# Kernel tuning notes

Measured on AMD Instinct MI355X. Metric: run time of the kernel, lower is better.

The kernel has to match this reference:

```python
import jax, jax.numpy as jnp
import numpy as np

B, L, D, K = 4, 512, 768, 96
H = 4 * D  # projection hidden width


def _proj(x, w1, b1, w2, b2):
    # create_projection_layer: Linear -> ReLU -> (Dropout, identity at eval) -> Linear
    return jnp.maximum(x @ w1 + b1, 0.0) @ w2 + b2


def setup_inputs() -> dict:
    key = jax.random.key(0)
    ks = jax.random.split(key, 12)
    g = lambda k, shape, fan: jax.random.normal(k, shape, jnp.float32) * (1.0 / np.sqrt(fan))
    inp = {
        "h": jax.random.normal(ks[0], (B, L, D), jnp.float32),
        "span_idx": jax.random.randint(ks[1], (B, K, 2), 0, L),
        "ps_w1": g(ks[2], (D, H), D), "ps_b1": jnp.zeros((H,), jnp.float32),
        "ps_w2": g(ks[3], (H, D), H), "ps_b2": jnp.zeros((D,), jnp.float32),
        "pe_w1": g(ks[4], (D, H), D), "pe_b1": jnp.zeros((H,), jnp.float32),
        "pe_w2": g(ks[5], (H, D), H), "pe_b2": jnp.zeros((D,), jnp.float32),
        "so_w1": g(ks[6], (2 * D, H), 2 * D), "so_b1": jnp.zeros((H,), jnp.float32),
        "so_w2": g(ks[7], (H, D), H), "so_b2": jnp.zeros((D,), jnp.float32),
        "ro_w1": g(ks[8], (2 * D, H), 2 * D), "ro_b1": jnp.zeros((H,), jnp.float32),
        "ro_w2": g(ks[9], (H, D), H), "ro_b2": jnp.zeros((D,), jnp.float32),
    }
    return inp


def _gather_tokens(rep, idx):
    # rep: [B,L,D], idx: [B,K] -> [B,K,D]
    b, k = idx.shape
    d = rep.shape[-1]
    return jnp.take_along_axis(rep, jnp.broadcast_to(idx[:, :, None], (b, k, d)), axis=1)


def reference(h, span_idx, ps_w1, ps_b1, ps_w2, ps_b2, pe_w1, pe_b1, pe_w2, pe_b2,
              so_w1, so_b1, so_w2, so_b2, ro_w1, ro_b1, ro_w2, ro_b2):
    # SpanMarkerV1
    start_rep = _proj(h, ps_w1, ps_b1, ps_w2, ps_b2)   # [B,L,D]
    end_rep = _proj(h, pe_w1, pe_b1, pe_w2, pe_b2)     # [B,L,D]
    st = _gather_tokens(start_rep, span_idx[:, :, 0])  # [B,K,D]
    en = _gather_tokens(end_rep, span_idx[:, :, 1])    # [B,K,D]
    cat = jnp.maximum(jnp.concatenate([st, en], axis=-1), 0.0)  # relu
    entity_reps = _proj(cat, so_w1, so_b1, so_w2, so_b2)        # [B,K,D]

    # off-diagonal pair enumeration, row-major (i,j) with i != j — static indices
    n = entity_reps.shape[1]
    idx = np.arange(n)
    ii = np.repeat(idx, n)
    jj = np.tile(idx, n)
    keep = ii != jj
    ii, jj = ii[keep], jj[keep]  # each length n*(n-1)
    pairs = jnp.concatenate([entity_reps[:, ii], entity_reps[:, jj]], axis=-1)  # [B,P,2D]
    return _proj(pairs, ro_w1, ro_b1, ro_w2, ro_b2)  # [B,P,D]
```

## Files before the change

### kernel.cpp

```cpp
#include <hip/hip_runtime.h>
#include <hip/hip_bf16.h>

#define Bdim 4
#define Ldim 512
#define Ddim 768
#define Kspan 96
#define Hdim 3072
#define Pdim 9120
#define MROWS 384
#define NT6 96

typedef __bf16 bf16x8 __attribute__((ext_vector_type(8)));
typedef float f32x4 __attribute__((ext_vector_type(4)));
typedef float f32x16 __attribute__((ext_vector_type(16)));
typedef unsigned short ushort8v __attribute__((ext_vector_type(8)));
typedef unsigned int uint4v __attribute__((ext_vector_type(4)));

static __device__ __forceinline__ unsigned short f2bf(float x){
  return __builtin_bit_cast(unsigned short, (__bf16)x);
}
static __device__ __forceinline__ float bf2f(unsigned short u){
  return (float)__builtin_bit_cast(__bf16, u);
}

struct TJob { const float* W; unsigned short* Th; unsigned short* Tl; int K; int N; int base; };
struct TJobs { TJob j[7]; };

__global__ __launch_bounds__(256) void transpose_multi(TJobs JJ)
{
  int x = blockIdx.x;
  int ji = 0;
  #pragma unroll
  for (int q = 1; q < 7; q++) if (x >= JJ.j[q].base) ji = q;
  TJob J = JJ.j[ji];
  int local = x - J.base;
  int tilesX = J.N >> 6;
  int bx = local % tilesX, by = local / tilesX;
  __shared__ float tile[64][65];
  int k0 = by * 64, n0 = bx * 64;
  int c = threadIdx.x & 63, r0 = threadIdx.x >> 6;
  for (int p = 0; p < 16; p++){
    int r = r0 + p * 4;
    tile[c][r] = J.W[(size_t)(k0 + r) * J.N + n0 + c];
  }
  __syncthreads();
  for (int p = 0; p < 16; p++){
    int n = r0 + p * 4;
    float xv = tile[n][c];
    unsigned short h = f2bf(xv);
    size_t o = (size_t)(n0 + n) * J.K + k0 + c;
    J.Th[o] = h;
    J.Tl[o] = f2bf(xv - bf2f(h));
  }
}

__global__ __launch_bounds__(256) void pack_w2(
    const float* __restrict__ W, unsigned short* __restrict__ W2B)
{
  __shared__ float tile[32][129];
  int kt = blockIdx.x, nq = blockIdx.y, t = threadIdx.x;
  for (int q = 0; q < 16; q++){
    int flat = q * 256 + t;
    int kl = flat >> 7, n = flat & 127;
    tile[kl][n] = W[(size_t)(kt * 32 + kl) * Ddim + nq * 128 + n];
  }
  __syncthreads();
  unsigned short* outp = W2B + (size_t)(nq * 96 + kt) * 4096;
  for (int q = 0; q < 16; q++){
    int o = q * 256 + t;
    int wn = (o >> 11) & 1, kh = (o >> 10) & 1, nf = (o >> 9) & 1;
    int hs = (o >> 8) & 1, l31 = (o >> 3) & 31, e = o & 7;
    int nl = wn * 64 + nf * 32 + l31;
    int kl = (kh * 2 + hs) * 8 + e;
    outp[o] = f2bf(tile[kl][nl]);
  }
}

__global__ __launch_bounds__(256) void pack_v_frag(
    const unsigned short* __restrict__ Vb, unsigned short* __restrict__ Vpk)
{
  int kt = blockIdx.x, b = blockIdx.y, t = threadIdx.x;
  unsigned short* outp = Vpk + (size_t)(b * 96 + kt) * 3072;
  #pragma unroll
  for (int q = 0; q < 12; q++){
    int o = q * 256 + t;
    int kh = o / 1536;
    int rem = o - kh * 1536;
    int mf = rem >> 9;
    int rem2 = rem & 511;
    int hsel = rem2 >> 8, l31 = (rem2 >> 3) & 31, e = rem2 & 7;
    outp[o] = Vb[(size_t)(b * 96 + mf * 32 + l31) * Hdim + kt * 32 + (kh * 2 + hsel) * 8 + e];
  }
}

__global__ __launch_bounds__(256) void gather_rows(
    const float* __restrict__ h, const int* __restrict__ span, float* __restrict__ hg)
{
  int x = blockIdx.x;
  int sel = (x >= MROWS) ? 1 : 0;
  int r = x - sel * MROWS;
  int b = r / Kspan, k = r - b * Kspan;
  int idx = span[(b * Kspan + k) * 2 + sel];
  const float* src = h + ((size_t)b * Ldim + idx) * Ddim;
  float* dst = hg + (size_t)x * Ddim;
  for (int d = threadIdx.x; d < Ddim; d += 256) dst[d] = src[d];
}

struct GJob {
  const float* A;
  const unsigned short* Wh;
  const unsigned short* Wl;
  const float* bias;
  float* C;
};

template<int MODE, int SPLIT>
__global__ __launch_bounds__(256) void gemm_ms(
    GJob j0, GJob j1, int ldA, int ldW, int ldC, int kLen, size_t csz)
{
  constexpr int SR = 40;
  __shared__ __align__(16) unsigned short Ah[64 * SR], Al[64 * SR];
  __shared__ __align__(16) unsigned short Bh[128 * SR], Bl[128 * SR];
  int zj, s;
  if (SPLIT == 1){ zj = blockIdx.z; s = 0; }
  else { zj = blockIdx.z / SPLIT; s = blockIdx.z % SPLIT; }
  const GJob J = zj ? j1 : j0;
  int kBegin = s * kLen;
  float* Cptr = (MODE == 2) ? (J.C + (size_t)s * csz) : J.C;

  int m0 = blockIdx.y * 64, n0 = blockIdx.x * 128;
  int t = threadIdx.x, lane = t & 63, wid = t >> 6;
  int wm = wid >> 1, wn = wid & 1;
  int lr = lane & 15, lk = (lane >> 4) * 8;
  f32x4 acc[2][4] = {};
  int ar = t >> 2, akq = t & 3;
  for (int k0 = 0; k0 < kLen; k0 += 32){
    {
      const float* sp = J.A + (size_t)(m0 + ar) * ldA + kBegin + k0 + akq * 8;
      f32x4 x0 = *(const f32x4*)sp, x1 = *(const f32x4*)(sp + 4);
      ushort8v vh, vl;
      for (int e = 0; e < 4; e++){ float x = x0[e]; unsigned short hh = f2bf(x); vh[e] = hh; vl[e] = f2bf(x - bf2f(hh)); }
      for (int e = 0; e < 4; e++){ float x = x1[e]; unsigned short hh = f2bf(x); vh[e+4] = hh; vl[e+4] = f2bf(x - bf2f(hh)); }
      *(ushort8v*)&Ah[ar * SR + akq * 8] = vh;
      *(ushort8v*)&Al[ar * SR + akq * 8] = vl;
    }
    for (int p = 0; p < 2; p++){
      int idx = p * 256 + t; int n = idx >> 2, kq = idx & 3;
      size_t go = (size_t)(n0 + n) * ldW + kBegin + k0 + kq * 8;
      *(ushort8v*)&Bh[n * SR + kq * 8] = *(const ushort8v*)(J.Wh + go);
      *(ushort8v*)&Bl[n * SR + kq * 8] = *(const ushort8v*)(J.Wl + go);
    }
    __syncthreads();
    bf16x8 ah[2], al2[2], bh[4], bl[4];
    for (int f = 0; f < 2; f++){ int o = (wm * 32 + f * 16 + lr) * SR + lk; ah[f] = *(const bf16x8*)&Ah[o]; al2[f] = *(const bf16x8*)&Al[o]; }
    for (int g = 0; g < 4; g++){ int o = (wn * 64 + g * 16 + lr) * SR + lk; bh[g] = *(const bf16x8*)&Bh[o]; bl[g] = *(const bf16x8*)&Bl[o]; }
    for (int f = 0; f < 2; f++)
      for (int g = 0; g < 4; g++){
        acc[f][g] = __builtin_amdgcn_mfma_f32_16x16x32_bf16(ah[f],  bh[g], acc[f][g], 0, 0, 0);
        acc[f][g] = __builtin_amdgcn_mfma_f32_16x16x32_bf16(ah[f],  bl[g], acc[f][g], 0, 0, 0);
        acc[f][g] = __builtin_amdgcn_mfma_f32_16x16x32_bf16(al2[f], bh[g], acc[f][g], 0, 0, 0);
      }
    __syncthreads();
  }
  int rr = (lane >> 4) * 4;
  for (int f = 0; f < 2; f++){
    int gm = m0 + wm * 32 + f * 16 + rr;
    for (int g = 0; g < 4; g++){
      int gn = n0 + wn * 64 + g * 16 + (lane & 15);
      float bv = (MODE != 2 && J.bias) ? J.bias[gn] : 0.f;
      for (int r2 = 0; r2 < 4; r2++){
        float v = acc[f][g][r2] + bv;
        if (MODE == 0) v = fmaxf(v, 0.f);
        if (MODE == 6){
          ((unsigned short*)J.C)[(size_t)(gm + r2) * ldC + gn] = f2bf(v);
        } else {
          Cptr[(size_t)(gm + r2) * ldC + gn] = v;
        }
      }
    }
  }
}

template<bool RELU>
__global__ __launch_bounds__(256) void reduce_part(
    const float* __restrict__ P, int S,
    const float* __restrict__ bias0, const float* __restrict__ bias1,
    float* __restrict__ outp, int zCount, int ldOut)
{
  const int MN = MROWS * Ddim;
  int idx4 = blockIdx.x * 256 + threadIdx.x;
  int flat = idx4 * 4;
  if (flat >= MN * zCount) return;
  int z = flat / MN; int rem = flat - z * MN;
  int r = rem / Ddim; int c = rem - r * Ddim;
  const float* base = P + (size_t)z * S * MN + rem;
  f32x4 sv = *(const f32x4*)base;
  for (int ss = 1; ss < S; ss++){ f32x4 v = *(const f32x4*)(base + (size_t)ss * MN); sv += v; }
  const float* bp = z ? bias1 : bias0;
  f32x4 bv = *(const f32x4*)(bp + c);
  sv += bv;
  if (RELU) for (int e = 0; e < 4; e++) sv[e] = fmaxf(sv[e], 0.f);
  *(f32x4*)(outp + (size_t)r * ldOut + z * Ddim + c) = sv;
}

__global__ __launch_bounds__(256, 2) void pair_gemm13(
    const unsigned short* __restrict__ Ub,
    const unsigned short* __restrict__ Vpk,
    const unsigned short* __restrict__ W2B,
    const float* __restrict__ b2,
    float* __restrict__ out)
{
  int x = blockIdx.x;
  int xcd = x & 7;
  int s = x >> 3;
  int grp = s / 48;
  int ig  = s - grp * 48;
  int combo = xcd + grp * 8;
  int nq = combo % 6, b = combo / 6;

  int t = threadIdx.x, lane = t & 63, w = t >> 6;
  int wm = w >> 1, wn = w & 1;
  int l31 = lane & 31, hsel = lane >> 5;
  int i = ig * 2 + wm;

  f32x16 acc[3][2] = {};

  const unsigned short* Vt = Vpk + (size_t)(b * 96) * 3072 + lane * 8;
  const unsigned short* Wt = W2B + (size_t)(nq * 96) * 4096 + wn * 2048 + lane * 8;
  const unsigned short* Ut = Ub + (size_t)(b * 96 + i) * Hdim + hsel * 8;

  ushort8v vE0, vE1, vE2, vE3, vE4, vE5, uE0, uE1;
  ushort8v vO0, vO1, vO2, vO3, vO4, vO5, uO0, uO1;

  #define LOADV_(KT, V0, V1, V2, V3, V4, V5) { \
    const unsigned short* p_ = Vt + (size_t)(KT) * 3072; \
    V0 = *(const ushort8v*)(p_);        V1 = *(const ushort8v*)(p_ + 512); \
    V2 = *(const ushort8v*)(p_ + 1024); V3 = *(const ushort8v*)(p_ + 1536); \
    V4 = *(const ushort8v*)(p_ + 2048); V5 = *(const ushort8v*)(p_ + 2560); \
  }
  #define LOADU_(KT, U0, U1) { \
    const unsigned short* p_ = Ut + (KT) * 32; \
    U0 = *(const ushort8v*)(p_); U1 = *(const ushort8v*)(p_ + 16); \
  }

  auto mkfrag = [](ushort8v v, ushort8v u) -> bf16x8 {
    bf16x8 sv2 = __builtin_bit_cast(bf16x8, v) + __builtin_bit_cast(bf16x8, u);
    bf16x8 z = {};
    return __builtin_elementwise_max(sv2, z);
  };

  LOADV_(0, vE0, vE1, vE2, vE3, vE4, vE5);
  LOADU_(0, uE0, uE1);

  for (int kt = 0; kt < NT6; kt += 2){
    {
      const unsigned short* wp = Wt + (size_t)kt * 4096;
      ushort8v b0 = *(const ushort8v*)(wp);
      ushort8v b1 = *(const ushort8v*)(wp + 512);
      ushort8v b2v = *(const ushort8v*)(wp + 1024);
      ushort8v b3 = *(const ushort8v*)(wp + 1536);
      LOADV_(kt + 1, vO0, vO1, vO2, vO3, vO4, vO5);
      LOADU_(kt + 1, uO0, uO1);
      bf16x8 a;
      a = mkfrag(vE0, uE0);
      acc[0][0] = __builtin_amdgcn_mfma_f32_32x32x16_bf16(a, __builtin_bit_cast(bf16x8, b0), acc[0][0], 0, 0, 0);
      acc[0][1] = __builtin_amdgcn_mfma_f32_32x32x16_bf16(a, __builtin_bit_cast(bf16x8, b1), acc[0][1], 0, 0, 0);
      a = mkfrag(vE1, uE0);
      acc[1][0] = __builtin_amdgcn_mfma_f32_32x32x16_bf16(a, __builtin_bit_cast(bf16x8, b0), acc[1][0], 0, 0, 0);
      acc[1][1] = __builtin_amdgcn_mfma_f32_32x32x16_bf16(a, __builtin_bit_cast(bf16x8, b1), acc[1][1], 0, 0, 0);
      a = mkfrag(vE2, uE0);
      acc[2][0] = __builtin_amdgcn_mfma_f32_32x32x16_bf16(a, __builtin_bit_cast(bf16x8, b0), acc[2][0], 0, 0, 0);
      acc[2][1] = __builtin_amdgcn_mfma_f32_32x32x16_bf16(a, __builtin_bit_cast(bf16x8, b1), acc[2][1], 0, 0, 0);
      a = mkfrag(vE3, uE1);
      acc[0][0] = __builtin_amdgcn_mfma_f32_32x32x16_bf16(a, __builtin_bit_cast(bf16x8, b2v), acc[0][0], 0, 0, 0);
      acc[0][1] = __builtin_amdgcn_mfma_f32_32x32x16_bf16(a, __builtin_bit_cast(bf16x8, b3), acc[0][1], 0, 0, 0);
      a = mkfrag(vE4, uE1);
      acc[1][0] = __builtin_amdgcn_mfma_f32_32x32x16_bf16(a, __builtin_bit_cast(bf16x8, b2v), acc[1][0], 0, 0, 0);
      acc[1][1] = __builtin_amdgcn_mfma_f32_32x32x16_bf16(a, __builtin_bit_cast(bf16x8, b3), acc[1][1], 0, 0, 0);
      a = mkfrag(vE5, uE1);
      acc[2][0] = __builtin_amdgcn_mfma_f32_32x32x16_bf16(a, __builtin_bit_cast(bf16x8, b2v), acc[2][0], 0, 0, 0);
      acc[2][1] = __builtin_amdgcn_mfma_f32_32x32x16_bf16(a, __builtin_bit_cast(bf16x8, b3), acc[2][1], 0, 0, 0);
    }
    {
      int ko = kt + 1;
      const unsigned short* wp = Wt + (size_t)ko * 4096;
      ushort8v b0 = *(const ushort8v*)(wp);
      ushort8v b1 = *(const ushort8v*)(wp + 512);
      ushort8v b2v = *(const ushort8v*)(wp + 1024);
      ushort8v b3 = *(const ushort8v*)(wp + 1536);
      if (ko + 1 < NT6){
        LOADV_(ko + 1, vE0, vE1, vE2, vE3, vE4, vE5);
        LOADU_(ko + 1, uE0, uE1);
      }
      bf16x8 a;
      a = mkfrag(vO0, uO0);
      acc[0][0] = __builtin_amdgcn_mfma_f32_32x32x16_bf16(a, __builtin_bit_cast(bf16x8, b0), acc[0][0], 0, 0, 0);
      acc[0][1] = __builtin_amdgcn_mfma_f32_32x32x16_bf16(a, __builtin_bit_cast(bf16x8, b1), acc[0][1], 0, 0, 0);
      a = mkfrag(vO1, uO0);
      acc[1][0] = __builtin_amdgcn_mfma_f32_32x32x16_bf16(a, __builtin_bit_cast(bf16x8, b0), acc[1][0], 0, 0, 0);
      acc[1][1] = __builtin_amdgcn_mfma_f32_32x32x16_bf16(a, __builtin_bit_cast(bf16x8, b1), acc[1][1], 0, 0, 0);
      a = mkfrag(vO2, uO0);
      acc[2][0] = __builtin_amdgcn_mfma_f32_32x32x16_bf16(a, __builtin_bit_cast(bf16x8, b0), acc[2][0], 0, 0, 0);
      acc[2][1] = __builtin_amdgcn_mfma_f32_32x32x16_bf16(a, __builtin_bit_cast(bf16x8, b1), acc[2][1], 0, 0, 0);
      a = mkfrag(vO3, uO1);
      acc[0][0] = __builtin_amdgcn_mfma_f32_32x32x16_bf16(a, __builtin_bit_cast(bf16x8, b2v), acc[0][0], 0, 0, 0);
      acc[0][1] = __builtin_amdgcn_mfma_f32_32x32x16_bf16(a, __builtin_bit_cast(bf16x8, b3), acc[0][1], 0, 0, 0);
      a = mkfrag(vO4, uO1);
      acc[1][0] = __builtin_amdgcn_mfma_f32_32x32x16_bf16(a, __builtin_bit_cast(bf16x8, b2v), acc[1][0], 0, 0, 0);
      acc[1][1] = __builtin_amdgcn_mfma_f32_32x32x16_bf16(a, __builtin_bit_cast(bf16x8, b3), acc[1][1], 0, 0, 0);
      a = mkfrag(vO5, uO1);
      acc[2][0] = __builtin_amdgcn_mfma_f32_32x32x16_bf16(a, __builtin_bit_cast(bf16x8, b2v), acc[2][0], 0, 0, 0);
      acc[2][1] = __builtin_amdgcn_mfma_f32_32x32x16_bf16(a, __builtin_bit_cast(bf16x8, b3), acc[2][1], 0, 0, 0);
    }
  }
  #undef LOADV_
  #undef LOADU_

  size_t outB = (size_t)b * Pdim;
  int colbase = nq * 128 + wn * 64;
  float bc[2];
  #pragma unroll
  for (int nf = 0; nf < 2; nf++) bc[nf] = b2[colbase + nf * 32 + l31];
  #pragma unroll
  for (int mf = 0; mf < 3; mf++){
    #pragma unroll
    for (int reg = 0; reg < 16; reg++){
      int j = mf * 32 + (reg & 3) + 8 * (reg >> 2) + 4 * hsel;
      if (j == i) continue;
      int p = i * 95 + j - (j > i ? 1 : 0);
      float* orow = out + (outB + p) * Ddim + colbase;
      #pragma unroll
      for (int nf = 0; nf < 2; nf++)
        orow[nf * 32 + l31] = acc[mf][nf][reg] + bc[nf];
    }
  }
}

extern "C" void kernel_launch(void* const* d_in, const int* in_sizes, int n_in,
                              void* d_out, int out_size, void* d_ws, size_t ws_size,
                              hipStream_t stream)
{
  (void)in_sizes; (void)n_in; (void)out_size;
  const float* h     = (const float*)d_in[0];
  const int*   span  = (const int*)d_in[1];
  const float* ps_w1 = (const float*)d_in[2];
  const float* ps_b1 = (const float*)d_in[3];
  const float* ps_w2 = (const float*)d_in[4];
  const float* ps_b2 = (const float*)d_in[5];
  const float* pe_w1 = (const float*)d_in[6];
  const float* pe_b1 = (const float*)d_in[7];
  const float* pe_w2 = (const float*)d_in[8];
  const float* pe_b2 = (const float*)d_in[9];
  const float* so_w1 = (const float*)d_in[10];
  const float* so_b1 = (const float*)d_in[11];
  const float* so_w2 = (const float*)d_in[12];
  const float* so_b2 = (const float*)d_in[13];
  const float* ro_w1 = (const float*)d_in[14];
  const float* ro_b1 = (const float*)d_in[15];
  const float* ro_w2 = (const float*)d_in[16];
  const float* ro_b2 = (const float*)d_in[17];

  char* ws = (char*)d_ws;
  size_t off = 0;
  auto alloc_us = [&](size_t n)->unsigned short*{
    unsigned short* p = (unsigned short*)(ws + off);
    off += ((n * 2 + 255) & ~(size_t)255);
    return p;
  };
  auto alloc_f = [&](size_t n)->float*{
    float* p = (float*)(ws + off);
    off += ((n * 4 + 255) & ~(size_t)255);
    return p;
  };

  unsigned short* ps1h = alloc_us((size_t)Hdim * Ddim); unsigned short* ps1l = alloc_us((size_t)Hdim * Ddim);
  unsigned short* ps2h = alloc_us((size_t)Ddim * Hdim); unsigned short* ps2l = alloc_us((size_t)Ddim * Hdim);
  unsigned short* pe1h = alloc_us((size_t)Hdim * Ddim); unsigned short* pe1l = alloc_us((size_t)Hdim * Ddim);
  unsigned short* pe2h = alloc_us((size_t)Ddim * Hdim); unsigned short* pe2l = alloc_us((size_t)Ddim * Hdim);
  unsigned short* so1h = alloc_us((size_t)Hdim * 2 * Ddim); unsigned short* so1l = alloc_us((size_t)Hdim * 2 * Ddim);
  unsigned short* so2h = alloc_us((size_t)Ddim * Hdim); unsigned short* so2l = alloc_us((size_t)Ddim * Hdim);
  unsigned short* ro1h = alloc_us((size_t)Hdim * 2 * Ddim); unsigned short* ro1l = alloc_us((size_t)Hdim * 2 * Ddim);
  unsigned short* W2B  = alloc_us((size_t)6 * 96 * 4096);
  unsigned short* Vp   = alloc_us((size_t)MROWS * Hdim);
  unsigned short* Ubf  = alloc_us((size_t)MROWS * Hdim);
  unsigned short* Vpk  = alloc_us((size_t)MROWS * Hdim);
  float* hg     = alloc_f((size_t)2 * MROWS * Ddim);
  float* mid_s  = alloc_f((size_t)MROWS * Hdim);
  float* mid_e  = alloc_f((size_t)MROWS * Hdim);
  float* cat    = alloc_f((size_t)MROWS * 2 * Ddim);
  float* entity = alloc_f((size_t)MROWS * Ddim);
  const size_t MN = (size_t)MROWS * Ddim;
  float* P2 = alloc_f(8 * MN);
  float* P3 = alloc_f(8 * MN);
  if (off > ws_size) return;

  dim3 tb(256);

  {
    TJobs JJ;
    int base = 0;
    auto add = [&](int idx, const float* W, unsigned short* Th, unsigned short* Tl, int K, int N){
      JJ.j[idx] = TJob{W, Th, Tl, K, N, base};
      base += (N / 64) * (K / 64);
    };
    add(0, ps_w1, ps1h, ps1l, Ddim, Hdim);
    add(1, ps_w2, ps2h, ps2l, Hdim, Ddim);
    add(2, pe_w1, pe1h, pe1l, Ddim, Hdim);
    add(3, pe_w2, pe2h, pe2l, Hdim, Ddim);
    add(4, so_w1, so1h, so1l, 2 * Ddim, Hdim);
    add(5, so_w2, so2h, so2l, Hdim, Ddim);
    add(6, ro_w1, ro1h, ro1l, 2 * Ddim, Hdim);
    transpose_multi<<<base, tb, 0, stream>>>(JJ);
  }
  pack_w2<<<dim3(NT6, 6), tb, 0, stream>>>(ro_w2, W2B);

  gather_rows<<<2 * MROWS, tb, 0, stream>>>(h, span, hg);

  {
    GJob j0{hg,                      ps1h, ps1l, ps_b1, mid_s};
    GJob j1{hg + (size_t)MROWS*Ddim, pe1h, pe1l, pe_b1, mid_e};
    gemm_ms<0,1><<<dim3(Hdim/128, MROWS/64, 2), tb, 0, stream>>>(j0, j1, Ddim, Ddim, Hdim, Ddim, 0);
  }
  {
    GJob j0{mid_s, ps2h, ps2l, nullptr, P2};
    GJob j1{mid_e, pe2h, pe2l, nullptr, P2 + 4*MN};
    gemm_ms<2,4><<<dim3(Ddim/128, MROWS/64, 8), tb, 0, stream>>>(j0, j1, Hdim, Hdim, Ddim, Hdim/4, MN);
  }
  reduce_part<true><<<(2*(int)MN)/1024, tb, 0, stream>>>(P2, 4, ps_b2, pe_b2, cat, 2, 2*Ddim);
  {
    GJob j0{cat, so1h, so1l, so_b1, mid_s};
    gemm_ms<0,1><<<dim3(Hdim/128, MROWS/64, 1), tb, 0, stream>>>(j0, j0, 2*Ddim, 2*Ddim, Hdim, 2*Ddim, 0);
  }
  {
    GJob j0{mid_s, so2h, so2l, nullptr, P3};
    gemm_ms<2,8><<<dim3(Ddim/128, MROWS/64, 8), tb, 0, stream>>>(j0, j0, Hdim, Hdim, Ddim, Hdim/8, MN);
  }
  reduce_part<false><<<((int)MN)/1024, tb, 0, stream>>>(P3, 8, so_b2, so_b2, entity, 1, Ddim);
  {
    GJob j0{entity, ro1h,        ro1l,        ro_b1,  (float*)Ubf};
    GJob j1{entity, ro1h + Ddim, ro1l + Ddim, nullptr, (float*)Vp};
    gemm_ms<6,1><<<dim3(Hdim/128, MROWS/64, 2), tb, 0, stream>>>(j0, j1, Ddim, 2*Ddim, Hdim, Ddim, 0);
  }
  pack_v_frag<<<dim3(NT6, Bdim), tb, 0, stream>>>(Vp, Vpk);

  pair_gemm13<<<1152, tb, 0, stream>>>(Ubf, Vpk, W2B, ro_b2, (float*)d_out);
}
```

Baseline: 534.0 us.

## Widen pair GEMM tile to full output row per block, repack W2

The pair GEMM now gives each block one entity row i for one batch. Its four waves each cover 192 output columns, so one block produces the full 768-column width instead of splitting across 6 column quarters. This reuses the relu(U+V) A-fragment across 6 N-fragments, cutting repeated V/U loads and fragment construction, and pack_w2 is re-laid out to match. The fragment builder also switches to explicit fp32 add/max with a packed bf16 convert. The trade-off is 18 accumulator tiles per wave (higher register pressure, occupancy 1) and only 384 blocks on the device.

```diff
diff --git a/kernel.cpp b/kernel.cpp
--- a/kernel.cpp
+++ b/kernel.cpp
@@ -57,22 +57,24 @@
 __global__ __launch_bounds__(256) void pack_w2(
     const float* __restrict__ W, unsigned short* __restrict__ W2B)
 {
-  __shared__ float tile[32][129];
-  int kt = blockIdx.x, nq = blockIdx.y, t = threadIdx.x;
-  for (int q = 0; q < 16; q++){
+  __shared__ float tile[32][193];
+  int kt = blockIdx.x, wq = blockIdx.y, t = threadIdx.x;
+  for (int q = 0; q < 24; q++){
     int flat = q * 256 + t;
-    int kl = flat >> 7, n = flat & 127;
-    tile[kl][n] = W[(size_t)(kt * 32 + kl) * Ddim + nq * 128 + n];
+    int kl = flat / 192, n = flat - kl * 192;
+    tile[kl][n] = W[(size_t)(kt * 32 + kl) * Ddim + wq * 192 + n];
   }
   __syncthreads();
-  unsigned short* outp = W2B + (size_t)(nq * 96 + kt) * 4096;
-  for (int q = 0; q < 16; q++){
+  unsigned short* outp = W2B + (size_t)kt * 24576 + wq * 6144;
+  for (int q = 0; q < 24; q++){
     int o = q * 256 + t;
-    int wn = (o >> 11) & 1, kh = (o >> 10) & 1, nf = (o >> 9) & 1;
-    int hs = (o >> 8) & 1, l31 = (o >> 3) & 31, e = o & 7;
-    int nl = wn * 64 + nf * 32 + l31;
+    int nf = o >> 10;
+    int r2 = o & 1023;
+    int kh = r2 >> 9;
+    int r3 = r2 & 511;
+    int hs = (r3 >> 8) & 1, l31 = (r3 >> 3) & 31, e = r3 & 7;
     int kl = (kh * 2 + hs) * 8 + e;
-    outp[o] = f2bf(tile[kl][nl]);
+    outp[o] = f2bf(tile[kl][nf * 32 + l31]);
   }
 }
 
@@ -203,7 +205,7 @@
   *(f32x4*)(outp + (size_t)r * ldOut + z * Ddim + c) = sv;
 }
 
-__global__ __launch_bounds__(256, 2) void pair_gemm13(
+__global__ __launch_bounds__(256, 1) void pair_gemm14(
     const unsigned short* __restrict__ Ub,
     const unsigned short* __restrict__ Vpk,
     const unsigned short* __restrict__ W2B,
@@ -213,20 +215,16 @@
   int x = blockIdx.x;
   int xcd = x & 7;
   int s = x >> 3;
-  int grp = s / 48;
-  int ig  = s - grp * 48;
-  int combo = xcd + grp * 8;
-  int nq = combo % 6, b = combo / 6;
+  int b = xcd >> 1;
+  int i = (xcd & 1) * 48 + s;
 
   int t = threadIdx.x, lane = t & 63, w = t >> 6;
-  int wm = w >> 1, wn = w & 1;
   int l31 = lane & 31, hsel = lane >> 5;
-  int i = ig * 2 + wm;
-
-  f32x16 acc[3][2] = {};
+
+  f32x16 acc[3][6] = {};
 
   const unsigned short* Vt = Vpk + (size_t)(b * 96) * 3072 + lane * 8;
-  const unsigned short* Wt = W2B + (size_t)(nq * 96) * 4096 + wn * 2048 + lane * 8;
+  const unsigned short* Wt = W2B + w * 6144 + lane * 8;
   const unsigned short* Ut = Ub + (size_t)(b * 96 + i) * Hdim + hsel * 8;
 
   ushort8v vE0, vE1, vE2, vE3, vE4, vE5, uE0, uE1;
@@ -242,85 +240,88 @@
     const unsigned short* p_ = Ut + (KT) * 32; \
     U0 = *(const ushort8v*)(p_); U1 = *(const ushort8v*)(p_ + 16); \
   }
+  #define LOADB_(KT, BB) { \
+    const unsigned short* p_ = Wt + (size_t)(KT) * 24576; \
+    _Pragma("unroll") \
+    for (int nf_ = 0; nf_ < 6; nf_++){ \
+      BB[nf_ * 2 + 0] = *(const ushort8v*)(p_ + nf_ * 1024); \
+      BB[nf_ * 2 + 1] = *(const ushort8v*)(p_ + nf_ * 1024 + 512); \
+    } \
+  }
 
   auto mkfrag = [](ushort8v v, ushort8v u) -> bf16x8 {
-    bf16x8 sv2 = __builtin_bit_cast(bf16x8, v) + __builtin_bit_cast(bf16x8, u);
-    bf16x8 z = {};
-    return __builtin_elementwise_max(sv2, z);
+    uint4v va = __builtin_bit_cast(uint4v, v);
+    uint4v ua = __builtin_bit_cast(uint4v, u);
+    uint4v po;
+    #pragma unroll
+    for (int j = 0; j < 4; j++){
+      float f0 = __builtin_bit_cast(float, va[j] << 16);
+      float f1 = __builtin_bit_cast(float, va[j] & 0xFFFF0000u);
+      float g0 = __builtin_bit_cast(float, ua[j] << 16);
+      float g1 = __builtin_bit_cast(float, ua[j] & 0xFFFF0000u);
+      float s0 = fmaxf(f0 + g0, 0.f);
+      float s1 = fmaxf(f1 + g1, 0.f);
+      unsigned int pk_;
+      asm("v_cvt_pk_bf16_f32 %0, %1, %2" : "=v"(pk_) : "v"(s0), "v"(s1));
+      po[j] = pk_;
+    }
+    return __builtin_bit_cast(bf16x8, po);
   };
+
+  #define TILE_(VV0, VV1, VV2, VV3, VV4, VV5, UU0, UU1, BB) { \
+    bf16x8 a_; \
+    a_ = mkfrag(VV0, UU0); \
+    _Pragma("unroll") \
+    for (int nf = 0; nf < 6; nf++) acc[0][nf] = __builtin_amdgcn_mfma_f32_32x32x16_bf16(a_, __builtin_bit_cast(bf16x8, BB[nf*2+0]), acc[0][nf], 0, 0, 0); \
+    a_ = mkfrag(VV1, UU0); \
+    _Pragma("unroll") \
+    for (int nf = 0; nf < 6; nf++) acc[1][nf] = __builtin_amdgcn_mfma_f32_32x32x16_bf16(a_, __builtin_bit_cast(bf16x8, BB[nf*2+0]), acc[1][nf], 0, 0, 0); \
+    a_ = mkfrag(VV2, UU0); \
+    _Pragma("unroll") \
+    for (int nf = 0; nf < 6; nf++) acc[2][nf] = __builtin_amdgcn_mfma_f32_32x32x16_bf16(a_, __builtin_bit_cast(bf16x8, BB[nf*2+0]), acc[2][nf], 0, 0, 0); \
+    a_ = mkfrag(VV3, UU1); \
+    _Pragma("unroll") \
+    for (int nf = 0; nf < 6; nf++) acc[0][nf] = __builtin_amdgcn_mfma_f32_32x32x16_bf16(a_, __builtin_bit_cast(bf16x8, BB[nf*2+1]), acc[0][nf], 0, 0, 0); \
+    a_ = mkfrag(VV4, UU1); \
+    _Pragma("unroll") \
+    for (int nf = 0; nf < 6; nf++) acc[1][nf] = __builtin_amdgcn_mfma_f32_32x32x16_bf16(a_, __builtin_bit_cast(bf16x8, BB[nf*2+1]), acc[1][nf], 0, 0, 0); \
+    a_ = mkfrag(VV5, UU1); \
+    _Pragma("unroll") \
+    for (int nf = 0; nf < 6; nf++) acc[2][nf] = __builtin_amdgcn_mfma_f32_32x32x16_bf16(a_, __builtin_bit_cast(bf16x8, BB[nf*2+1]), acc[2][nf], 0, 0, 0); \
+  }
 
   LOADV_(0, vE0, vE1, vE2, vE3, vE4, vE5);
   LOADU_(0, uE0, uE1);
 
   for (int kt = 0; kt < NT6; kt += 2){
     {
-      const unsigned short* wp = Wt + (size_t)kt * 4096;
-      ushort8v b0 = *(const ushort8v*)(wp);
-      ushort8v b1 = *(const ushort8v*)(wp + 512);
-      ushort8v b2v = *(const ushort8v*)(wp + 1024);
-      ushort8v b3 = *(const ushort8v*)(wp + 1536);
+      ushort8v bb[12];
+      LOADB_(kt, bb);
       LOADV_(kt + 1, vO0, vO1, vO2, vO3, vO4, vO5);
       LOADU_(kt + 1, uO0, uO1);
-      bf16x8 a;
-      a = mkfrag(vE0, uE0);
-      acc[0][0] = __builtin_amdgcn_mfma_f32_32x32x16_bf16(a, __builtin_bit_cast(bf16x8, b0), acc[0][0], 0, 0, 0);
-      acc[0][1] = __builtin_amdgcn_mfma_f32_32x32x16_bf16(a, __builtin_bit_cast(bf16x8, b1), acc[0][1], 0, 0, 0);
-      a = mkfrag(vE1, uE0);
-      acc[1][0] = __builtin_amdgcn_mfma_f32_32x32x16_bf16(a, __builtin_bit_cast(bf16x8, b0), acc[1][0], 0, 0, 0);
-      acc[1][1] = __builtin_amdgcn_mfma_f32_32x32x16_bf16(a, __builtin_bit_cast(bf16x8, b1), acc[1][1], 0, 0, 0);
-      a = mkfrag(vE2, uE0);
-      acc[2][0] = __builtin_amdgcn_mfma_f32_32x32x16_bf16(a, __builtin_bit_cast(bf16x8, b0), acc[2][0], 0, 0, 0);
-      acc[2][1] = __builtin_amdgcn_mfma_f32_32x32x16_bf16(a, __builtin_bit_cast(bf16x8, b1), acc[2][1], 0, 0, 0);
-      a = mkfrag(vE3, uE1);
-      acc[0][0] = __builtin_amdgcn_mfma_f32_32x32x16_bf16(a, __builtin_bit_cast(bf16x8, b2v), acc[0][0], 0, 0, 0);
-      acc[0][1] = __builtin_amdgcn_mfma_f32_32x32x16_bf16(a, __builtin_bit_cast(bf16x8, b3), acc[0][1], 0, 0, 0);
-      a = mkfrag(vE4, uE1);
-      acc[1][0] = __builtin_amdgcn_mfma_f32_32x32x16_bf16(a, __builtin_bit_cast(bf16x8, b2v), acc[1][0], 0, 0, 0);
-      acc[1][1] = __builtin_amdgcn_mfma_f32_32x32x16_bf16(a, __builtin_bit_cast(bf16x8, b3), acc[1][1], 0, 0, 0);
-      a = mkfrag(vE5, uE1);
-      acc[2][0] = __builtin_amdgcn_mfma_f32_32x32x16_bf16(a, __builtin_bit_cast(bf16x8, b2v), acc[2][0], 0, 0, 0);
-      acc[2][1] = __builtin_amdgcn_mfma_f32_32x32x16_bf16(a, __builtin_bit_cast(bf16x8, b3), acc[2][1], 0, 0, 0);
+      TILE_(vE0, vE1, vE2, vE3, vE4, vE5, uE0, uE1, bb)
     }
     {
       int ko = kt + 1;
-      const unsigned short* wp = Wt + (size_t)ko * 4096;
-      ushort8v b0 = *(const ushort8v*)(wp);
-      ushort8v b1 = *(const ushort8v*)(wp + 512);
-      ushort8v b2v = *(const ushort8v*)(wp + 1024);
-      ushort8v b3 = *(const ushort8v*)(wp + 1536);
+      ushort8v bb[12];
+      LOADB_(ko, bb);
       if (ko + 1 < NT6){
         LOADV_(ko + 1, vE0, vE1, vE2, vE3, vE4, vE5);
         LOADU_(ko + 1, uE0, uE1);
       }
-      bf16x8 a;
-      a = mkfrag(vO0, uO0);
-      acc[0][0] = __builtin_amdgcn_mfma_f32_32x32x16_bf16(a, __builtin_bit_cast(bf16x8, b0), acc[0][0], 0, 0, 0);
-      acc[0][1] = __builtin_amdgcn_mfma_f32_32x32x16_bf16(a, __builtin_bit_cast(bf16x8, b1), acc[0][1], 0, 0, 0);
-      a = mkfrag(vO1, uO0);
-      acc[1][0] = __builtin_amdgcn_mfma_f32_32x32x16_bf16(a, __builtin_bit_cast(bf16x8, b0), acc[1][0], 0, 0, 0);
-      acc[1][1] = __builtin_amdgcn_mfma_f32_32x32x16_bf16(a, __builtin_bit_cast(bf16x8, b1), acc[1][1], 0, 0, 0);
-      a = mkfrag(vO2, uO0);
-      acc[2][0] = __builtin_amdgcn_mfma_f32_32x32x16_bf16(a, __builtin_bit_cast(bf16x8, b0), acc[2][0], 0, 0, 0);
-      acc[2][1] = __builtin_amdgcn_mfma_f32_32x32x16_bf16(a, __builtin_bit_cast(bf16x8, b1), acc[2][1], 0, 0, 0);
-      a = mkfrag(vO3, uO1);
-      acc[0][0] = __builtin_amdgcn_mfma_f32_32x32x16_bf16(a, __builtin_bit_cast(bf16x8, b2v), acc[0][0], 0, 0, 0);
-      acc[0][1] = __builtin_amdgcn_mfma_f32_32x32x16_bf16(a, __builtin_bit_cast(bf16x8, b3), acc[0][1], 0, 0, 0);
-      a = mkfrag(vO4, uO1);
-      acc[1][0] = __builtin_amdgcn_mfma_f32_32x32x16_bf16(a, __builtin_bit_cast(bf16x8, b2v), acc[1][0], 0, 0, 0);
-      acc[1][1] = __builtin_amdgcn_mfma_f32_32x32x16_bf16(a, __builtin_bit_cast(bf16x8, b3), acc[1][1], 0, 0, 0);
-      a = mkfrag(vO5, uO1);
-      acc[2][0] = __builtin_amdgcn_mfma_f32_32x32x16_bf16(a, __builtin_bit_cast(bf16x8, b2v), acc[2][0], 0, 0, 0);
-      acc[2][1] = __builtin_amdgcn_mfma_f32_32x32x16_bf16(a, __builtin_bit_cast(bf16x8, b3), acc[2][1], 0, 0, 0);
+      TILE_(vO0, vO1, vO2, vO3, vO4, vO5, uO0, uO1, bb)
     }
   }
   #undef LOADV_
   #undef LOADU_
+  #undef LOADB_
+  #undef TILE_
 
   size_t outB = (size_t)b * Pdim;
-  int colbase = nq * 128 + wn * 64;
-  float bc[2];
+  int colbase = w * 192;
+  float bc[6];
   #pragma unroll
-  for (int nf = 0; nf < 2; nf++) bc[nf] = b2[colbase + nf * 32 + l31];
+  for (int nf = 0; nf < 6; nf++) bc[nf] = b2[colbase + nf * 32 + l31];
   #pragma unroll
   for (int mf = 0; mf < 3; mf++){
     #pragma unroll
@@ -330,7 +331,7 @@
       int p = i * 95 + j - (j > i ? 1 : 0);
       float* orow = out + (outB + p) * Ddim + colbase;
       #pragma unroll
-      for (int nf = 0; nf < 2; nf++)
+      for (int nf = 0; nf < 6; nf++)
         orow[nf * 32 + l31] = acc[mf][nf][reg] + bc[nf];
     }
   }
@@ -380,7 +381,7 @@
   unsigned short* so1h = alloc_us((size_t)Hdim * 2 * Ddim); unsigned short* so1l = alloc_us((size_t)Hdim * 2 * Ddim);
   unsigned short* so2h = alloc_us((size_t)Ddim * Hdim); unsigned short* so2l = alloc_us((size_t)Ddim * Hdim);
   unsigned short* ro1h = alloc_us((size_t)Hdim * 2 * Ddim); unsigned short* ro1l = alloc_us((size_t)Hdim * 2 * Ddim);
-  unsigned short* W2B  = alloc_us((size_t)6 * 96 * 4096);
+  unsigned short* W2B  = alloc_us((size_t)96 * 24576);
   unsigned short* Vp   = alloc_us((size_t)MROWS * Hdim);
   unsigned short* Ubf  = alloc_us((size_t)MROWS * Hdim);
   unsigned short* Vpk  = alloc_us((size_t)MROWS * Hdim);
@@ -412,7 +413,7 @@
     add(6, ro_w1, ro1h, ro1l, 2 * Ddim, Hdim);
     transpose_multi<<<base, tb, 0, stream>>>(JJ);
   }
-  pack_w2<<<dim3(NT6, 6), tb, 0, stream>>>(ro_w2, W2B);
+  pack_w2<<<dim3(NT6, 4), tb, 0, stream>>>(ro_w2, W2B);
 
   gather_rows<<<2 * MROWS, tb, 0, stream>>>(h, span, hg);
 
@@ -443,5 +444,5 @@
   }
   pack_v_frag<<<dim3(NT6, Bdim), tb, 0, stream>>>(Vp, Vpk);
 
-  pair_gemm13<<<1152, tb, 0, stream>>>(Ubf, Vpk, W2B, ro_b2, (float*)d_out);
-}
+  pair_gemm14<<<384, tb, 0, stream>>>(Ubf, Vpk, W2B, ro_b2, (float*)d_out);
+}
```

Result: slower. 1.486 ms (+178.2%).
